# Performance work log

Hardware: AMD Instinct MI355X
Metric: run time of the kernel (lower is better)

## Reference

```python
import jax, jax.numpy as jnp
import numpy as np

THETA = 10000.0

def _rope(x, cos, sin):
    # x: [B, S, D]; cos/sin: [S, D/2]. Pairs are (x[..., 2i], x[..., 2i+1]) treated as complex.
    xr = x.reshape(*x.shape[:-1], -1, 2)
    x0, x1 = xr[..., 0], xr[..., 1]
    o0 = x0 * cos - x1 * sin
    o1 = x0 * sin + x1 * cos
    return jnp.stack([o0, o1], axis=-1).reshape(x.shape)

def setup_inputs() -> dict:
    key = jax.random.key(0)
    ks = jax.random.split(key, 7)
    B, S, D = 4, 2048, 1024
    sd = 1.0 / np.sqrt(D)
    return {
        "x": jax.random.normal(ks[0], (B, S, D), dtype=jnp.float32),
        "wq_w": jax.random.normal(ks[1], (D, D), dtype=jnp.float32) * sd,
        "wq_b": jax.random.normal(ks[2], (D,), dtype=jnp.float32) * 0.01,
        "wk_w": jax.random.normal(ks[3], (D, D), dtype=jnp.float32) * sd,
        "wk_b": jax.random.normal(ks[4], (D,), dtype=jnp.float32) * 0.01,
        "wv_w": jax.random.normal(ks[5], (D, D), dtype=jnp.float32) * sd,
        "wv_b": jax.random.normal(ks[6], (D,), dtype=jnp.float32) * 0.01,
    }

def reference(x, wq_w, wq_b, wk_w, wk_b, wv_w, wv_b):
    B, S, D = x.shape
    # QKV projections (torch Linear: y = x @ W.T + b)
    q = jnp.einsum('bsd,ed->bse', x, wq_w) + wq_b
    k = jnp.einsum('bsd,ed->bse', x, wk_w) + wk_b
    v = jnp.einsum('bsd,ed->bse', x, wv_w) + wv_b
    # Rotary embedding: freqs_cis[t, i] = exp(i * t / theta^(2i/D))
    inv_freq = 1.0 / (THETA ** (jnp.arange(0, D, 2, dtype=jnp.float32) / D))  # [D/2]
    ang = jnp.arange(S, dtype=jnp.float32)[:, None] * inv_freq[None, :]  # [S, D/2]
    cos, sin = jnp.cos(ang), jnp.sin(ang)
    q = _rope(q, cos, sin)
    k = _rope(k, cos, sin)
    # Full (non-causal, single-head) attention with scale 1/sqrt(dim)
    scores = jnp.einsum('bqd,bkd->bqk', q, k) / jnp.sqrt(jnp.float32(D))
    probs = jax.nn.softmax(scores.astype(jnp.float32), axis=-1)
    return jnp.einsum('bqk,bkd->bqd', probs, v)
```

## Files before the change

### kernel.cpp

```cpp
#include <hip/hip_runtime.h>
#include <cstdint>

using u16 = unsigned short;
using u32 = unsigned int;

typedef __attribute__((ext_vector_type(8))) short short8;
typedef __attribute__((ext_vector_type(4))) float floatx4;

__device__ __forceinline__ u16 f2bf(float f) {
    u32 u = __float_as_uint(f);
    u32 r = u + 0x7fffu + ((u >> 16) & 1u);
    return (u16)(r >> 16);
}

__global__ void cvt_all(const float* __restrict__ x, u16* __restrict__ xb,
                        const float* __restrict__ w0, const float* __restrict__ w1,
                        const float* __restrict__ w2,
                        u16* __restrict__ o0, u16* __restrict__ o1, u16* __restrict__ o2,
                        const float* __restrict__ qb, const float* __restrict__ kb,
                        float* __restrict__ bqk, float* __restrict__ rowsum)
{
    int b = blockIdx.x;
    if (b >= 11272) {
        long i = ((long)(b - 11272) * 256 + threadIdx.x) * 4;
        *reinterpret_cast<float4*>(rowsum + i) = make_float4(0.f, 0.f, 0.f, 0.f);
        return;
    }
    if (b >= 11264) {
        int i = (b - 11264) * 256 + threadIdx.x;
        bqk[i] = (i < 1024) ? qb[i] : kb[i - 1024];
        return;
    }
    const float* src; u16* dst; long base;
    if (b < 8192) { src = x; dst = xb; base = (long)b; }
    else {
        int r = b - 8192, seg = r >> 10;
        if (seg == 0)      { src = w0; dst = o0; }
        else if (seg == 1) { src = w1; dst = o1; }
        else               { src = w2; dst = o2; }
        base = (long)(r & 1023);
    }
    long i = (base * 256 + threadIdx.x) * 4;
    float4 v = *reinterpret_cast<const float4*>(src + i);
    uint2 o;
    o.x = (u32)f2bf(v.x) | ((u32)f2bf(v.y) << 16);
    o.y = (u32)f2bf(v.z) | ((u32)f2bf(v.w) << 16);
    *reinterpret_cast<uint2*>(dst + i) = o;
}

__device__ __forceinline__ void async_cp16(const u16* g, u16* l) {
    __builtin_amdgcn_global_load_lds(
        (const __attribute__((address_space(1))) void*)g,
        (__attribute__((address_space(3))) void*)l, 16, 0, 0);
}

#define MEMFENCE asm volatile("" ::: "memory")
__device__ __forceinline__ void barrier_raw() {
    MEMFENCE; __builtin_amdgcn_s_barrier(); MEMFENCE;
}
__device__ __forceinline__ void vmwait(int n) {
    if      (n == 6) asm volatile("s_waitcnt vmcnt(6)" ::: "memory");
    else if (n == 4) asm volatile("s_waitcnt vmcnt(4)" ::: "memory");
    else if (n == 2) asm volatile("s_waitcnt vmcnt(2)" ::: "memory");
    else if (n == 0) asm volatile("s_waitcnt vmcnt(0)" ::: "memory");
}

template <bool BF16_OUT, bool EXPOUT>
__device__ __forceinline__ void gemm8_core(
    const u16* __restrict__ A, const u16* __restrict__ B, void* __restrict__ Cv,
    int K, int lda, int ldb, int ldc,
    long tile_m, long tile_n, long cbase,
    const float* __restrict__ bias_col, const float* __restrict__ bias_row,
    float scale, bool rope, float* __restrict__ rowsum, u16* smem)
{
    const int tid  = threadIdx.x;
    const int lane = tid & 63;
    const int wave = tid >> 6;
    const int wm2  = (wave >> 2) * 128;
    const int wn2  = (wave & 3) * 64;
    const int fm   = lane & 15;
    const int fks  = (((lane >> 4) ^ ((lane >> 1) & 3))) * 8;

    const int srow = tid >> 2;
    const int kgl  = ((tid & 3) ^ ((tid >> 3) & 3)) * 8;
    const u16* Asrc = A + (tile_m + srow) * (long)lda + kgl;
    const u16* Bsrc = B + (tile_n + srow) * (long)ldb + kgl;
    u16* dst0 = smem + tid * 8;

    const int U = K >> 5;

    floatx4 acc[8][4] = {};
    short8 bf[4];

    auto stageA = [&](int v) {
        u16* d = dst0 + ((2 * v) & 7) * 8192;
        const u16* s = Asrc + v * 32;
        async_cp16(s, d);
        async_cp16(s + 128 * (long)lda, d + 4096);
    };
    auto stageB = [&](int v) {
        u16* d = dst0 + ((2 * v + 1) & 7) * 8192;
        const u16* s = Bsrc + v * 32;
        async_cp16(s, d);
        async_cp16(s + 128 * (long)ldb, d + 4096);
    };

    auto phase_pair = [&](int u, int vmx, bool stb, bool sta)
        __attribute__((always_inline))
    {
        const u16* Ap = smem + ((2 * u) & 7) * 8192;
        const u16* Bp = smem + ((2 * u + 1) & 7) * 8192;
        short8 af[4];
        #pragma unroll
        for (int i = 0; i < 4; ++i)
            af[i] = *reinterpret_cast<const short8*>(&Ap[(wm2 + i * 16 + fm) * 32 + fks]);
        #pragma unroll
        for (int j = 0; j < 4; ++j)
            bf[j] = *reinterpret_cast<const short8*>(&Bp[(wn2 + j * 16 + fm) * 32 + fks]);
        if (stb) stageB(u + 2);
        vmwait(vmx);
        barrier_raw();
        __builtin_amdgcn_sched_barrier(0);
        __builtin_amdgcn_s_setprio(1);
        #pragma unroll
        for (int i = 0; i < 4; ++i)
            #pragma unroll
            for (int j = 0; j < 4; ++j)
                acc[i][j] = __builtin_amdgcn_mfma_f32_16x16x32_bf16(af[i], bf[j], acc[i][j], 0, 0, 0);
        __builtin_amdgcn_s_setprio(0);
        __builtin_amdgcn_sched_barrier(0);
        barrier_raw();
        #pragma unroll
        for (int i = 0; i < 4; ++i)
            af[i] = *reinterpret_cast<const short8*>(&Ap[(wm2 + 64 + i * 16 + fm) * 32 + fks]);
        if (sta) stageA(u + 3);
        barrier_raw();
        __builtin_amdgcn_sched_barrier(0);
        __builtin_amdgcn_s_setprio(1);
        #pragma unroll
        for (int i = 0; i < 4; ++i)
            #pragma unroll
            for (int j = 0; j < 4; ++j)
                acc[4 + i][j] = __builtin_amdgcn_mfma_f32_16x16x32_bf16(af[i], bf[j], acc[4 + i][j], 0, 0, 0);
        __builtin_amdgcn_s_setprio(0);
        __builtin_amdgcn_sched_barrier(0);
        barrier_raw();
    };

    stageA(0); stageB(0); stageA(1); stageB(1); stageA(2);
    vmwait(6);
    barrier_raw();

    for (int u = 0; u + 3 < U; ++u)
        phase_pair(u, 6, true, true);
    phase_pair(U - 3, 6, true,  false);
    phase_pair(U - 2, 2, false, false);
    phase_pair(U - 1, 0, false, false);

    const int q4  = lane >> 4;
    const int c16 = lane & 15;
    float* smemf  = (float*)smem;
    float* myeps  = smemf + wave * (16 * 68);
    const long n0 = tile_n + wn2 + c16 * 4;

    float4 bc4 = make_float4(0.f, 0.f, 0.f, 0.f);
    if (bias_col) bc4 = *reinterpret_cast<const float4*>(bias_col + n0);

    float inv0 = 0.f, inv1 = 0.f;
    if (rope) {
        int p0 = (int)(n0 >> 1);
        inv0 = __expf((float)(p0 & 511)       * -1.79889463e-2f);
        inv1 = __expf((float)((p0 + 1) & 511) * -1.79889463e-2f);
    }

    #pragma unroll
    for (int i = 0; i < 8; ++i) {
        #pragma unroll
        for (int j = 0; j < 4; ++j)
            #pragma unroll
            for (int r = 0; r < 4; ++r)
                myeps[(q4 * 4 + r) * 68 + j * 16 + c16] = acc[i][j][r];
        __syncthreads();
        #pragma unroll
        for (int p = 0; p < 4; ++p) {
            int lrow = p * 4 + q4;
            long m = tile_m + wm2 + i * 16 + lrow;
            float4 v = *reinterpret_cast<const float4*>(&myeps[lrow * 68 + c16 * 4]);
            v.x = v.x * scale + bc4.x;
            v.y = v.y * scale + bc4.y;
            v.z = v.z * scale + bc4.z;
            v.w = v.w * scale + bc4.w;
            if (bias_row) {
                float br = bias_row[m];
                v.x += br; v.y += br; v.z += br; v.w += br;
            }
            if (rope) {
                int s = (int)(m & 2047);
                float a0 = (float)s * inv0, a1 = (float)s * inv1;
                float sn0 = __sinf(a0), cs0 = __cosf(a0);
                float sn1 = __sinf(a1), cs1 = __cosf(a1);
                float x0 = v.x, x1 = v.y, x2 = v.z, x3 = v.w;
                v.x = x0 * cs0 - x1 * sn0;
                v.y = x0 * sn0 + x1 * cs0;
                v.z = x2 * cs1 - x3 * sn1;
                v.w = x2 * sn1 + x3 * cs1;
            }
            if constexpr (EXPOUT) {
                v.x = __expf(v.x); v.y = __expf(v.y);
                v.z = __expf(v.z); v.w = __expf(v.w);
                float s4 = v.x + v.y + v.z + v.w;
                s4 += __shfl_xor(s4, 1);
                s4 += __shfl_xor(s4, 2);
                s4 += __shfl_xor(s4, 4);
                s4 += __shfl_xor(s4, 8);
                if (c16 == 0) atomicAdd(&rowsum[m], s4);
            }
            long off = cbase + m * (long)ldc + n0;
            if constexpr (BF16_OUT) {
                uint2 o;
                o.x = (u32)f2bf(v.x) | ((u32)f2bf(v.y) << 16);
                o.y = (u32)f2bf(v.z) | ((u32)f2bf(v.w) << 16);
                *reinterpret_cast<uint2*>((u16*)Cv + off) = o;
            } else {
                *reinterpret_cast<float4*>((float*)Cv + off) = v;
            }
        }
        __syncthreads();
    }
}

__global__ __launch_bounds__(512, 2)
void gemm8_fused12(const u16* __restrict__ xb, const u16* __restrict__ wqk,
                   const u16* __restrict__ wv, u16* __restrict__ QK, u16* __restrict__ VT,
                   const float* __restrict__ bqk, const float* __restrict__ wvb)
{
    u32 id = blockIdx.x;
    id = (id & 7u) * 48u + (id >> 3);
    __shared__ alignas(16) u16 smem[65536];
    if (id < 256u) {
        u32 bx = id & 7u, by = id >> 3;
        gemm8_core<true, false>(xb, wqk, QK, 1024, 1024, 1024, 2048,
                                (long)by * 256, (long)bx * 256, 0L,
                                bqk, nullptr, 1.0f, true, nullptr, smem);
    } else {
        u32 r = id - 256u;
        u32 bz = r >> 5, q = r & 31u, bx = q & 7u, by = q >> 3;
        gemm8_core<true, false>(wv, xb + (long)bz * 2048 * 1024, VT,
                                1024, 1024, 1024, 2048,
                                (long)by * 256, (long)bx * 256, (long)bz * 1024 * 2048,
                                nullptr, wvb, 1.0f, false, nullptr, smem);
    }
}

__global__ __launch_bounds__(512, 2)
void gemm8_qkt(const u16* __restrict__ QK, u16* __restrict__ Pbuf,
               float* __restrict__ rsum)
{
    u32 id = blockIdx.x;
    id = (id & 7u) * 32u + (id >> 3);
    u32 bz = id >> 6, q = id & 63u, bx = q & 7u, by = q >> 3;
    __shared__ alignas(16) u16 smem[65536];
    const u16* base = QK + (long)bz * 2048 * 2048;
    gemm8_core<true, true>(base, base + 1024, Pbuf, 1024, 2048, 2048, 2048,
                           (long)by * 256, (long)bx * 256, (long)bz * 2048 * 2048,
                           nullptr, nullptr, 0.03125f, false,
                           rsum + (long)bz * 2048, smem);
}

template <bool BF16_OUT>
__device__ __forceinline__ void gemm_core_n64(
    const u16* __restrict__ A, const u16* __restrict__ B, void* __restrict__ Cv,
    int K, int lda, int ldb, int ldc,
    long tile_m, long tile_n, long cbase,
    float scale, const float* __restrict__ rowscale, u16* smem)
{
    u16* As = smem;
    u16* Bs = smem + 8192;

    const int tid  = threadIdx.x;
    const int lane = tid & 63;
    const int wave = tid >> 6;
    const int wm = (wave >> 1) << 6;
    const int wn = (wave & 1) << 5;

    floatx4 acc[4][2] = {};

    const int srow = tid >> 2;
    const int skp  = (((tid & 3) ^ (srow & 3))) * 8;
    const u16* Ag = A + (tile_m + srow) * (long)lda + skp;
    const u16* Bg = B + (tile_n + srow) * (long)ldb + skp;
    u16* Asl = &As[tid * 8];
    u16* Bsl = &Bs[tid * 8];

    const int fm  = lane & 15;
    const int fks = (((lane >> 4) ^ (lane & 3))) * 8;

    for (int k0 = 0; k0 < K; k0 += 64) {
        async_cp16(Ag,                       Asl);
        async_cp16(Ag + 64 * (long)lda,      Asl + 64 * 32);
        async_cp16(Ag + 32,                  Asl + 4096);
        async_cp16(Ag + 32 + 64 * (long)lda, Asl + 4096 + 64 * 32);
        async_cp16(Bg,                       Bsl);
        async_cp16(Bg + 32,                  Bsl + 2048);
        Ag += 64; Bg += 64;
        __syncthreads();

        #pragma unroll
        for (int c = 0; c < 2; ++c) {
            const u16* Ap = As + c * 4096;
            const u16* Bp = Bs + c * 2048;
            short8 af[4], bfr[2];
            #pragma unroll
            for (int i = 0; i < 4; ++i)
                af[i] = *reinterpret_cast<const short8*>(&Ap[(wm + i * 16 + fm) * 32 + fks]);
            #pragma unroll
            for (int j = 0; j < 2; ++j)
                bfr[j] = *reinterpret_cast<const short8*>(&Bp[(wn + j * 16 + fm) * 32 + fks]);
            #pragma unroll
            for (int i = 0; i < 4; ++i)
                #pragma unroll
                for (int j = 0; j < 2; ++j)
                    acc[i][j] = __builtin_amdgcn_mfma_f32_16x16x32_bf16(af[i], bfr[j], acc[i][j], 0, 0, 0);
        }
        __syncthreads();
    }

    const int q4  = lane >> 4;
    const int c16 = lane & 15;
    float* smemf = (float*)smem;
    float* myeps = smemf + wave * (16 * 36);
    const long n0 = tile_n + wn + c16 * 2;

    #pragma unroll
    for (int i = 0; i < 4; ++i) {
        #pragma unroll
        for (int j = 0; j < 2; ++j)
            #pragma unroll
            for (int r = 0; r < 4; ++r)
                myeps[(q4 * 4 + r) * 36 + j * 16 + c16] = acc[i][j][r];
        __syncthreads();
        #pragma unroll
        for (int p = 0; p < 4; ++p) {
            int lrow = p * 4 + q4;
            long m = tile_m + wm + i * 16 + lrow;
            float2 v = *reinterpret_cast<const float2*>(&myeps[lrow * 36 + c16 * 2]);
            float sc = scale;
            if (rowscale) sc *= 1.0f / rowscale[m];
            v.x *= sc; v.y *= sc;
            long off = cbase + m * (long)ldc + n0;
            if constexpr (BF16_OUT) {
                *reinterpret_cast<u32*>((u16*)Cv + off) =
                    (u32)f2bf(v.x) | ((u32)f2bf(v.y) << 16);
            } else {
                *reinterpret_cast<float2*>((float*)Cv + off) = v;
            }
        }
        __syncthreads();
    }
}

template <bool BF16_OUT>
__global__ __launch_bounds__(256)
void gemm_nt_n64(const u16* __restrict__ A, const u16* __restrict__ B, void* __restrict__ Cv,
                 int K, int lda, int ldb, int ldc,
                 long sA, long sB, long sC, float scale,
                 const float* __restrict__ rowscale)
{
    const u32 gx = gridDim.x, gy = gridDim.y;
    u32 id = blockIdx.x + gx * (blockIdx.y + gy * blockIdx.z);
    const u32 G = gx * gy * gridDim.z;
    if ((G & 7u) == 0u) id = (id & 7u) * (G >> 3) + (id >> 3);
    const u32 bx = id % gx;
    const u32 t1 = id / gx;
    const u32 by = t1 % gy;
    const u32 bz = t1 / gy;

    __shared__ alignas(16) u16 smem[12288];
    gemm_core_n64<BF16_OUT>(A + (long)bz * sA, B + (long)bz * sB, Cv,
                            K, lda, ldb, ldc,
                            (long)by * 128, (long)bx * 64, (long)bz * sC,
                            scale, rowscale ? rowscale + (long)bz * 2048 : nullptr, smem);
}

extern "C" void kernel_launch(void* const* d_in, const int* in_sizes, int n_in,
                              void* d_out, int out_size, void* d_ws, size_t ws_size,
                              hipStream_t stream)
{
    const float* x   = (const float*)d_in[0];
    const float* wqw = (const float*)d_in[1];
    const float* wqb = (const float*)d_in[2];
    const float* wkw = (const float*)d_in[3];
    const float* wkb = (const float*)d_in[4];
    const float* wvw = (const float*)d_in[5];
    const float* wvb = (const float*)d_in[6];
    float* out = (float*)d_out;

    char* ws = (char*)d_ws;
    const size_t MB = 1ull << 20;
    u16*   Pbuf = (u16*)(ws + 64 * MB);
    u16*   QK   = (u16*)(ws + 96 * MB);
    u16*   VT   = (u16*)(ws + 128 * MB);
    float* rsum = (float*)(ws + 144 * MB);
    u16*   xb    = (u16*)(ws + 0);
    u16*   wqk   = (u16*)(ws + 16 * MB);
    u16*   wvbuf = (u16*)(ws + 20 * MB);
    float* bqk   = (float*)(ws + 22 * MB);

    cvt_all<<<dim3(11280), 256, 0, stream>>>(x, xb, wqw, wkw, wvw,
                                             wqk, wqk + 1024 * 1024, wvbuf,
                                             wqb, wkb, bqk, rsum);

    gemm8_fused12<<<dim3(384), 512, 0, stream>>>(xb, wqk, wvbuf, QK, VT, bqk, wvb);

    gemm8_qkt<<<dim3(256), 512, 0, stream>>>(QK, Pbuf, rsum);

    gemm_nt_n64<false><<<dim3(16, 16, 4), 256, 0, stream>>>(
        Pbuf, VT, out, 2048, 2048, 2048, 1024,
        2048L * 2048, 1024L * 2048, 2048L * 1024, 1.0f, rsum);

    (void)in_sizes; (void)n_in; (void)out_size; (void)ws_size;
}
```

Before: 262.7 us.

## Use 128x128-tile 256-thread GEMM for QKV projection and PV product

```diff
diff --git a/kernel.cpp b/kernel.cpp
--- a/kernel.cpp
+++ b/kernel.cpp
@@ -63,6 +63,142 @@
     else if (n == 4) asm volatile("s_waitcnt vmcnt(4)" ::: "memory");
     else if (n == 2) asm volatile("s_waitcnt vmcnt(2)" ::: "memory");
     else if (n == 0) asm volatile("s_waitcnt vmcnt(0)" ::: "memory");
+}
+
+template <bool BF16_OUT, bool EXPOUT>
+__device__ __forceinline__ void gemm_core(
+    const u16* __restrict__ A, const u16* __restrict__ B, void* __restrict__ Cv,
+    int K, int lda, int ldb, int ldc,
+    long tile_m, long tile_n, long cbase,
+    const float* bias_col, const float* bias_row,
+    float scale, bool rope, float* __restrict__ rowsum,
+    const float* __restrict__ rowscale, u16* smem)
+{
+    u16* As = smem;
+    u16* Bs = smem + 8192;
+
+    const int tid  = threadIdx.x;
+    const int lane = tid & 63;
+    const int wave = tid >> 6;
+    const int wm = (wave >> 1) << 6;
+    const int wn = (wave & 1) << 6;
+
+    floatx4 acc[4][4] = {};
+
+    const int srow = tid >> 2;
+    const int skp  = (((tid & 3) ^ (srow & 3))) * 8;
+    const u16* Ag = A + (tile_m + srow) * (long)lda + skp;
+    const u16* Bg = B + (tile_n + srow) * (long)ldb + skp;
+    u16* Asl = &As[tid * 8];
+    u16* Bsl = &Bs[tid * 8];
+
+    const int fm  = lane & 15;
+    const int fks = (((lane >> 4) ^ (lane & 3))) * 8;
+
+    for (int k0 = 0; k0 < K; k0 += 64) {
+        async_cp16(Ag,                       Asl);
+        async_cp16(Ag + 64 * (long)lda,      Asl + 64 * 32);
+        async_cp16(Ag + 32,                  Asl + 4096);
+        async_cp16(Ag + 32 + 64 * (long)lda, Asl + 4096 + 64 * 32);
+        async_cp16(Bg,                       Bsl);
+        async_cp16(Bg + 64 * (long)ldb,      Bsl + 64 * 32);
+        async_cp16(Bg + 32,                  Bsl + 4096);
+        async_cp16(Bg + 32 + 64 * (long)ldb, Bsl + 4096 + 64 * 32);
+        Ag += 64; Bg += 64;
+        __syncthreads();
+
+        #pragma unroll
+        for (int c = 0; c < 2; ++c) {
+            const u16* Ap = As + c * 4096;
+            const u16* Bp = Bs + c * 4096;
+            short8 af[4], bfr[4];
+            #pragma unroll
+            for (int i = 0; i < 4; ++i)
+                af[i] = *reinterpret_cast<const short8*>(&Ap[(wm + i * 16 + fm) * 32 + fks]);
+            #pragma unroll
+            for (int j = 0; j < 4; ++j)
+                bfr[j] = *reinterpret_cast<const short8*>(&Bp[(wn + j * 16 + fm) * 32 + fks]);
+            #pragma unroll
+            for (int i = 0; i < 4; ++i)
+                #pragma unroll
+                for (int j = 0; j < 4; ++j)
+                    acc[i][j] = __builtin_amdgcn_mfma_f32_16x16x32_bf16(af[i], bfr[j], acc[i][j], 0, 0, 0);
+        }
+        __syncthreads();
+    }
+
+    const int q4  = lane >> 4;
+    const int c16 = lane & 15;
+    float* smemf  = (float*)smem;
+    float* myeps = smemf + wave * (16 * 68);
+    const long n0 = tile_n + wn + c16 * 4;
+
+    float4 bc4 = make_float4(0.f, 0.f, 0.f, 0.f);
+    if (bias_col) bc4 = *reinterpret_cast<const float4*>(bias_col + n0);
+
+    float inv0 = 0.f, inv1 = 0.f;
+    if (rope) {
+        int p0 = (int)(n0 >> 1);
+        inv0 = __expf((float)(p0 & 511)       * -1.79889463e-2f);
+        inv1 = __expf((float)((p0 + 1) & 511) * -1.79889463e-2f);
+    }
+
+    #pragma unroll
+    for (int i = 0; i < 4; ++i) {
+        #pragma unroll
+        for (int j = 0; j < 4; ++j)
+            #pragma unroll
+            for (int r = 0; r < 4; ++r)
+                myeps[(q4 * 4 + r) * 68 + j * 16 + c16] = acc[i][j][r];
+        __syncthreads();
+        #pragma unroll
+        for (int p = 0; p < 4; ++p) {
+            int lrow = p * 4 + q4;
+            long m = tile_m + wm + i * 16 + lrow;
+            float4 v = *reinterpret_cast<const float4*>(&myeps[lrow * 68 + c16 * 4]);
+            float sc = scale;
+            if (rowscale) sc *= 1.0f / rowscale[m];
+            v.x = v.x * sc + bc4.x;
+            v.y = v.y * sc + bc4.y;
+            v.z = v.z * sc + bc4.z;
+            v.w = v.w * sc + bc4.w;
+            if (bias_row) {
+                float br = bias_row[m];
+                v.x += br; v.y += br; v.z += br; v.w += br;
+            }
+            if (rope) {
+                int s = (int)(m & 2047);
+                float a0 = (float)s * inv0, a1 = (float)s * inv1;
+                float sn0 = __sinf(a0), cs0 = __cosf(a0);
+                float sn1 = __sinf(a1), cs1 = __cosf(a1);
+                float x0 = v.x, x1 = v.y, x2 = v.z, x3 = v.w;
+                v.x = x0 * cs0 - x1 * sn0;
+                v.y = x0 * sn0 + x1 * cs0;
+                v.z = x2 * cs1 - x3 * sn1;
+                v.w = x2 * sn1 + x3 * cs1;
+            }
+            if constexpr (EXPOUT) {
+                v.x = __expf(v.x); v.y = __expf(v.y);
+                v.z = __expf(v.z); v.w = __expf(v.w);
+                float s4 = v.x + v.y + v.z + v.w;
+                s4 += __shfl_xor(s4, 1);
+                s4 += __shfl_xor(s4, 2);
+                s4 += __shfl_xor(s4, 4);
+                s4 += __shfl_xor(s4, 8);
+                if (c16 == 0) atomicAdd(&rowsum[m], s4);
+            }
+            long off = cbase + m * (long)ldc + n0;
+            if constexpr (BF16_OUT) {
+                uint2 o;
+                o.x = (u32)f2bf(v.x) | ((u32)f2bf(v.y) << 16);
+                o.y = (u32)f2bf(v.z) | ((u32)f2bf(v.w) << 16);
+                *reinterpret_cast<uint2*>((u16*)Cv + off) = o;
+            } else {
+                *reinterpret_cast<float4*>((float*)Cv + off) = v;
+            }
+        }
+        __syncthreads();
+    }
 }
 
 template <bool BF16_OUT, bool EXPOUT>
@@ -229,26 +365,26 @@
     }
 }
 
-__global__ __launch_bounds__(512, 2)
-void gemm8_fused12(const u16* __restrict__ xb, const u16* __restrict__ wqk,
-                   const u16* __restrict__ wv, u16* __restrict__ QK, u16* __restrict__ VT,
-                   const float* __restrict__ bqk, const float* __restrict__ wvb)
+__global__ __launch_bounds__(256)
+void gemm_fused12(const u16* __restrict__ xb, const u16* __restrict__ wqk,
+                  const u16* __restrict__ wv, u16* __restrict__ QK, u16* __restrict__ VT,
+                  const float* __restrict__ bqk, const float* __restrict__ wvb)
 {
     u32 id = blockIdx.x;
-    id = (id & 7u) * 48u + (id >> 3);
-    __shared__ alignas(16) u16 smem[65536];
-    if (id < 256u) {
-        u32 bx = id & 7u, by = id >> 3;
-        gemm8_core<true, false>(xb, wqk, QK, 1024, 1024, 1024, 2048,
-                                (long)by * 256, (long)bx * 256, 0L,
-                                bqk, nullptr, 1.0f, true, nullptr, smem);
+    id = (id & 7u) * 192u + (id >> 3);
+    __shared__ alignas(16) u16 smem[16384];
+    if (id < 1024u) {
+        u32 bx = id & 15u, by = id >> 4;
+        gemm_core<true, false>(xb, wqk, QK, 1024, 1024, 1024, 2048,
+                        (long)by * 128, (long)bx * 128, 0L,
+                        bqk, nullptr, 1.0f, true, nullptr, nullptr, smem);
     } else {
-        u32 r = id - 256u;
-        u32 bz = r >> 5, q = r & 31u, bx = q & 7u, by = q >> 3;
-        gemm8_core<true, false>(wv, xb + (long)bz * 2048 * 1024, VT,
-                                1024, 1024, 1024, 2048,
-                                (long)by * 256, (long)bx * 256, (long)bz * 1024 * 2048,
-                                nullptr, wvb, 1.0f, false, nullptr, smem);
+        u32 r = id - 1024u;
+        u32 bx = r & 15u, by = (r >> 4) & 7u, bz = r >> 7;
+        gemm_core<true, false>(wv, xb + (long)bz * 2048 * 1024, VT,
+                        1024, 1024, 1024, 2048,
+                        (long)by * 128, (long)bx * 128, (long)bz * 1024 * 2048,
+                        nullptr, wvb, 1.0f, false, nullptr, nullptr, smem);
     }
 }
 
@@ -267,104 +403,13 @@
                            rsum + (long)bz * 2048, smem);
 }
 
-template <bool BF16_OUT>
-__device__ __forceinline__ void gemm_core_n64(
-    const u16* __restrict__ A, const u16* __restrict__ B, void* __restrict__ Cv,
-    int K, int lda, int ldb, int ldc,
-    long tile_m, long tile_n, long cbase,
-    float scale, const float* __restrict__ rowscale, u16* smem)
-{
-    u16* As = smem;
-    u16* Bs = smem + 8192;
-
-    const int tid  = threadIdx.x;
-    const int lane = tid & 63;
-    const int wave = tid >> 6;
-    const int wm = (wave >> 1) << 6;
-    const int wn = (wave & 1) << 5;
-
-    floatx4 acc[4][2] = {};
-
-    const int srow = tid >> 2;
-    const int skp  = (((tid & 3) ^ (srow & 3))) * 8;
-    const u16* Ag = A + (tile_m + srow) * (long)lda + skp;
-    const u16* Bg = B + (tile_n + srow) * (long)ldb + skp;
-    u16* Asl = &As[tid * 8];
-    u16* Bsl = &Bs[tid * 8];
-
-    const int fm  = lane & 15;
-    const int fks = (((lane >> 4) ^ (lane & 3))) * 8;
-
-    for (int k0 = 0; k0 < K; k0 += 64) {
-        async_cp16(Ag,                       Asl);
-        async_cp16(Ag + 64 * (long)lda,      Asl + 64 * 32);
-        async_cp16(Ag + 32,                  Asl + 4096);
-        async_cp16(Ag + 32 + 64 * (long)lda, Asl + 4096 + 64 * 32);
-        async_cp16(Bg,                       Bsl);
-        async_cp16(Bg + 32,                  Bsl + 2048);
-        Ag += 64; Bg += 64;
-        __syncthreads();
-
-        #pragma unroll
-        for (int c = 0; c < 2; ++c) {
-            const u16* Ap = As + c * 4096;
-            const u16* Bp = Bs + c * 2048;
-            short8 af[4], bfr[2];
-            #pragma unroll
-            for (int i = 0; i < 4; ++i)
-                af[i] = *reinterpret_cast<const short8*>(&Ap[(wm + i * 16 + fm) * 32 + fks]);
-            #pragma unroll
-            for (int j = 0; j < 2; ++j)
-                bfr[j] = *reinterpret_cast<const short8*>(&Bp[(wn + j * 16 + fm) * 32 + fks]);
-            #pragma unroll
-            for (int i = 0; i < 4; ++i)
-                #pragma unroll
-                for (int j = 0; j < 2; ++j)
-                    acc[i][j] = __builtin_amdgcn_mfma_f32_16x16x32_bf16(af[i], bfr[j], acc[i][j], 0, 0, 0);
-        }
-        __syncthreads();
-    }
-
-    const int q4  = lane >> 4;
-    const int c16 = lane & 15;
-    float* smemf = (float*)smem;
-    float* myeps = smemf + wave * (16 * 36);
-    const long n0 = tile_n + wn + c16 * 2;
-
-    #pragma unroll
-    for (int i = 0; i < 4; ++i) {
-        #pragma unroll
-        for (int j = 0; j < 2; ++j)
-            #pragma unroll
-            for (int r = 0; r < 4; ++r)
-                myeps[(q4 * 4 + r) * 36 + j * 16 + c16] = acc[i][j][r];
-        __syncthreads();
-        #pragma unroll
-        for (int p = 0; p < 4; ++p) {
-            int lrow = p * 4 + q4;
-            long m = tile_m + wm + i * 16 + lrow;
-            float2 v = *reinterpret_cast<const float2*>(&myeps[lrow * 36 + c16 * 2]);
-            float sc = scale;
-            if (rowscale) sc *= 1.0f / rowscale[m];
-            v.x *= sc; v.y *= sc;
-            long off = cbase + m * (long)ldc + n0;
-            if constexpr (BF16_OUT) {
-                *reinterpret_cast<u32*>((u16*)Cv + off) =
-                    (u32)f2bf(v.x) | ((u32)f2bf(v.y) << 16);
-            } else {
-                *reinterpret_cast<float2*>((float*)Cv + off) = v;
-            }
-        }
-        __syncthreads();
-    }
-}
-
-template <bool BF16_OUT>
+template <bool BF16_OUT, bool EXPOUT>
 __global__ __launch_bounds__(256)
-void gemm_nt_n64(const u16* __restrict__ A, const u16* __restrict__ B, void* __restrict__ Cv,
-                 int K, int lda, int ldb, int ldc,
-                 long sA, long sB, long sC, float scale,
-                 const float* __restrict__ rowscale)
+void gemm_nt(const u16* __restrict__ A, const u16* __restrict__ B, void* __restrict__ Cv,
+             int K, int lda, int ldb, int ldc,
+             long sA, long sB, long sC,
+             const float* __restrict__ bias_col, const float* __restrict__ bias_row,
+             float scale, float* __restrict__ rowsum, const float* __restrict__ rowscale)
 {
     const u32 gx = gridDim.x, gy = gridDim.y;
     u32 id = blockIdx.x + gx * (blockIdx.y + gy * blockIdx.z);
@@ -375,11 +420,13 @@
     const u32 by = t1 % gy;
     const u32 bz = t1 / gy;
 
-    __shared__ alignas(16) u16 smem[12288];
-    gemm_core_n64<BF16_OUT>(A + (long)bz * sA, B + (long)bz * sB, Cv,
-                            K, lda, ldb, ldc,
-                            (long)by * 128, (long)bx * 64, (long)bz * sC,
-                            scale, rowscale ? rowscale + (long)bz * 2048 : nullptr, smem);
+    __shared__ alignas(16) u16 smem[16384];
+    gemm_core<BF16_OUT, EXPOUT>(A + (long)bz * sA, B + (long)bz * sB, Cv,
+                        K, lda, ldb, ldc,
+                        (long)by * 128, (long)bx * 128, (long)bz * sC,
+                        bias_col, bias_row, scale, false,
+                        rowsum ? rowsum + (long)bz * 2048 : nullptr,
+                        rowscale ? rowscale + (long)bz * 2048 : nullptr, smem);
 }
 
 extern "C" void kernel_launch(void* const* d_in, const int* in_sizes, int n_in,
@@ -410,13 +457,14 @@
                                              wqk, wqk + 1024 * 1024, wvbuf,
                                              wqb, wkb, bqk, rsum);
 
-    gemm8_fused12<<<dim3(384), 512, 0, stream>>>(xb, wqk, wvbuf, QK, VT, bqk, wvb);
+    gemm_fused12<<<dim3(1536), 256, 0, stream>>>(xb, wqk, wvbuf, QK, VT, bqk, wvb);
 
     gemm8_qkt<<<dim3(256), 512, 0, stream>>>(QK, Pbuf, rsum);
 
-    gemm_nt_n64<false><<<dim3(16, 16, 4), 256, 0, stream>>>(
+    gemm_nt<false, false><<<dim3(8, 16, 4), 256, 0, stream>>>(
         Pbuf, VT, out, 2048, 2048, 2048, 1024,
-        2048L * 2048, 1024L * 2048, 2048L * 1024, 1.0f, rsum);
+        2048L * 2048, 1024L * 2048, 2048L * 1024,
+        nullptr, nullptr, 1.0f, nullptr, rsum);
 
     (void)in_sizes; (void)n_in; (void)out_size; (void)ws_size;
 }
```

Measured after the change: 250.2 us. -4.8%, faster.
